# Kernel tuning notes

Measured on AMD Instinct MI355X. Metric: run time of the kernel, lower is better.

The kernel has to match this reference:

```python
import jax, jax.numpy as jnp
import numpy as np

N, E, DIM, H = 50000, 800000, 64, 2
HD = H * DIM


def setup_inputs() -> dict:
    key = jax.random.key(0)
    ks = jax.random.split(key, 16)
    s = 0.05
    return {
        "x": jax.random.normal(ks[0], (N, DIM), jnp.float32),
        "edge_index": jax.random.randint(ks[1], (2, E), 0, N, jnp.int64),
        "Wq": jax.random.normal(ks[2], (DIM, HD), jnp.float32) * s,
        "bq": jax.random.normal(ks[3], (HD,), jnp.float32) * s,
        "Wk": jax.random.normal(ks[4], (DIM, HD), jnp.float32) * s,
        "bk": jax.random.normal(ks[5], (HD,), jnp.float32) * s,
        "Wv": jax.random.normal(ks[6], (DIM, HD), jnp.float32) * s,
        "bv": jax.random.normal(ks[7], (HD,), jnp.float32) * s,
        "Wskip": jax.random.normal(ks[8], (DIM, HD), jnp.float32) * s,
        "bskip": jax.random.normal(ks[9], (HD,), jnp.float32) * s,
        "Wc": jax.random.normal(ks[10], (HD, DIM), jnp.float32) * s,
        "bc": jax.random.normal(ks[11], (DIM,), jnp.float32) * s,
        "gamma": jnp.ones((DIM,), jnp.float32),
        "beta": jnp.zeros((DIM,), jnp.float32),
    }


def reference(x, edge_index, Wq, bq, Wk, bk, Wv, bv, Wskip, bskip, Wc, bc, gamma, beta):
    src, dst = edge_index[0], edge_index[1]  # messages flow src -> dst
    # TransformerConv: per-head q/k/v projections, [N, H, D]
    q = (x @ Wq + bq).reshape(N, H, DIM)
    k = (x @ Wk + bk).reshape(N, H, DIM)
    v = (x @ Wv + bv).reshape(N, H, DIM)
    scale = 1.0 / np.sqrt(DIM).astype(np.float32)
    # edge-wise attention logits: [E, H]
    alpha = jnp.einsum('ehd,ehd->eh', q[dst], k[src]) * scale
    # segment softmax over incoming edges of each dst node (PyG softmax)
    amax = jax.ops.segment_max(alpha, dst, num_segments=N)
    a = jnp.exp(alpha - amax[dst])
    asum = jax.ops.segment_sum(a, dst, num_segments=N)
    a = a / (asum[dst] + 1e-16)
    # weighted scatter-aggregate of values: [N, H, D] -> concat heads
    out = jax.ops.segment_sum(a[:, :, None] * v[src], dst, num_segments=N)
    out = out.reshape(N, HD)
    # root/skip connection (root_weight=True default)
    out = out + (x @ Wskip + bskip)
    # concat linear: H*D -> dim
    out = out @ Wc + bc
    # pyg.LayerNorm default mode='graph': normalize over ALL nodes+features
    out = out - out.mean()
    out = out / (out.std() + 1e-5)  # std with unbiased=False (jnp default ddof=0)
    return out * gamma + beta
```

## Files before the change

kernel.cpp:

```cpp
#include <hip/hip_runtime.h>
#include <hip/hip_bf16.h>

#define N_NODES 50000
#define N_EDGES 800000
#define DIM 64
#define NHEAD 2
#define HD 128
#define NCOL 448
#define MAXDEG 64

#define NBIN 196
#define BCAP 6144
#define ACH 2048
#define BIN_BLKS 391

#define PREP_B 112
#define PROJ_B 782

#define QSCALE 0.18033688011112042f

typedef short bf16x8 __attribute__((ext_vector_type(8)));
typedef float f32x16 __attribute__((ext_vector_type(16)));
typedef float f32x2 __attribute__((ext_vector_type(2)));

__device__ __forceinline__ unsigned short f2bf(float f) {
    unsigned u = __float_as_uint(f);
    unsigned r = (u + 0x7fffu + ((u >> 16) & 1u)) >> 16;
    return (unsigned short)r;
}
__device__ __forceinline__ unsigned char f2fp8(float f) {
    int r = __builtin_amdgcn_cvt_pk_fp8_f32(f, f, 0, false);
    return (unsigned char)(r & 0xff);
}

__global__ __launch_bounds__(256) void k_pb(
    const int* __restrict__ ei,
    const float* __restrict__ Wq, const float* __restrict__ bq,
    const float* __restrict__ Wk, const float* __restrict__ bk,
    const float* __restrict__ Wv, const float* __restrict__ bv,
    const float* __restrict__ Wskip, const float* __restrict__ bskip,
    const float* __restrict__ Wc, const float* __restrict__ bc,
    unsigned short* __restrict__ WallT, float* __restrict__ ball,
    int* __restrict__ bincnt, unsigned* __restrict__ bins,
    double* __restrict__ sacc)
{
    const int t = threadIdx.x;
    if (blockIdx.x < PREP_B) {
        if (blockIdx.x == 0) { sacc[t] = 0.0; sacc[256 + t] = 0.0; }
        int gid = blockIdx.x * 256 + t;
        const int j = gid >> 6;
        const int d = gid & 63;
        float w, bb;
        if (j < 128) {
            w = Wq[d * HD + j] * QSCALE;
            bb = bq[j] * QSCALE;
        } else if (j < 256) {
            int jj = j - 128;
            w = Wk[d * HD + jj];
            bb = bk[jj];
        } else if (j < 384) {
            int jj = j - 256;
            int h = jj >> 6, jc = jj & 63;
            float s = 0.f, sb = 0.f;
            for (int c = 0; c < 64; c++) {
                float wc = Wc[(h * 64 + c) * DIM + jc];
                s  += Wv[d * HD + h * 64 + c] * wc;
                sb += bv[h * 64 + c] * wc;
            }
            w = s; bb = sb;
        } else {
            int jj = j - 384;
            float s = 0.f, sb = bc[jj];
            for (int c = 0; c < HD; c++) {
                float wc = Wc[c * DIM + jj];
                s  += Wskip[d * HD + c] * wc;
                sb += bskip[c] * wc;
            }
            w = s; bb = sb;
        }
        WallT[gid] = f2bf(w);
        if (d == 0) ball[j] = bb;
        return;
    }
    __shared__ int hist[256];
    __shared__ int gbase[256];
    const int e0 = (blockIdx.x - PREP_B) * ACH;
    hist[t] = 0;
    __syncthreads();
    unsigned pk8[8];
    int bin8[8], sl8[8];
#pragma unroll
    for (int k = 0; k < 8; k++) {
        int e = e0 + t + k * 256;
        if (e < N_EDGES) {
            int src = ei[e];
            int d = ei[N_EDGES + e];
            int bin = d >> 8;
            pk8[k] = (unsigned)(((d & 255) << 16) | src);
            bin8[k] = bin;
            sl8[k] = atomicAdd(&hist[bin], 1);
        } else {
            bin8[k] = -1;
        }
    }
    __syncthreads();
    if (t < NBIN) {
        int h = hist[t];
        if (h > 0) gbase[t] = atomicAdd(&bincnt[t], h);
    }
    __syncthreads();
#pragma unroll
    for (int k = 0; k < 8; k++) {
        int bin = bin8[k];
        if (bin >= 0) {
            int pos = gbase[bin] + sl8[k];
            if (pos < BCAP) bins[(size_t)bin * BCAP + pos] = pk8[k];
        }
    }
}

__global__ __launch_bounds__(256) void k_ep(
    const float* __restrict__ x,
    const unsigned short* __restrict__ WallT, const float* __restrict__ ball,
    float* __restrict__ q, unsigned char* __restrict__ kv, float* __restrict__ skipc,
    const int* __restrict__ bincnt, const unsigned* __restrict__ bins,
    int* __restrict__ deg, unsigned short* __restrict__ elist)
{
    __shared__ __align__(16) unsigned char smem[65536];
    const int blk = blockIdx.x;
    const int t = threadIdx.x;
    if (blk >= PROJ_B) {
        const int bin = blk - PROJ_B;
        int* nodecnt = (int*)smem;
        nodecnt[t] = 0;
        __syncthreads();
        int cnt = bincnt[bin]; if (cnt > BCAP) cnt = BCAP;
        const unsigned* bp = bins + (size_t)bin * BCAP;
        for (int i = t; i < cnt; i += 256) {
            unsigned p = bp[i];
            int local = p >> 16;
            int src = p & 0xffff;
            int sl = atomicAdd(&nodecnt[local], 1);
            if (sl < MAXDEG)
                elist[((size_t)((bin << 8) | local)) * MAXDEG + sl] = (unsigned short)src;
        }
        __syncthreads();
        int node = (bin << 8) + t;
        if (node < N_NODES) {
            int dgv = nodecnt[t];
            deg[node] = dgv > MAXDEG ? MAXDEG : dgv;
        }
        return;
    }
    float* q_s = (float*)smem;
    unsigned char* kv_s = smem + 32768;
    float* sk_s = (float*)(smem + 49152);

    const int w = t >> 6;
    const int lane = t & 63;
    const int col = lane & 31;
    const int khalf = lane >> 5;
    const int nloc0 = (w >> 1) * 32;
    const int n0 = blk * 64 + nloc0;
    const int ct0 = (w & 1) * 7;
    const int rowbase = 4 * khalf;

    int nread = n0 + col; if (nread >= N_NODES) nread = N_NODES - 1;
    const float* ap = x + (size_t)nread * 64 + khalf * 8;
    bf16x8 afrag[4];
#pragma unroll
    for (int kk = 0; kk < 4; kk++) {
        float4 xa = *((const float4*)(ap + kk * 16));
        float4 xb4 = *((const float4*)(ap + kk * 16 + 4));
        bf16x8 f;
        f[0] = (short)f2bf(xa.x); f[1] = (short)f2bf(xa.y);
        f[2] = (short)f2bf(xa.z); f[3] = (short)f2bf(xa.w);
        f[4] = (short)f2bf(xb4.x); f[5] = (short)f2bf(xb4.y);
        f[6] = (short)f2bf(xb4.z); f[7] = (short)f2bf(xb4.w);
        afrag[kk] = f;
    }

    for (int tt = 0; tt < 7; tt++) {
        const int gc = (ct0 + tt) * 32 + col;
        const float b = ball[gc];
        f32x16 acc;
#pragma unroll
        for (int r = 0; r < 16; r++) acc[r] = b;
        const unsigned short* bp = WallT + (size_t)gc * 64 + khalf * 8;
#pragma unroll
        for (int kk = 0; kk < 4; kk++) {
            bf16x8 bfrag = *((const bf16x8*)(bp + kk * 16));
            acc = __builtin_amdgcn_mfma_f32_32x32x16_bf16(afrag[kk], bfrag, acc, 0, 0, 0);
        }
        if (gc < 128) {
#pragma unroll
            for (int r = 0; r < 16; r++) {
                int nl = nloc0 + rowbase + (r & 3) + 8 * (r >> 2);
                q_s[nl * 128 + gc] = acc[r];
            }
        } else if (gc < 384) {
            int ch = gc - 128;
            int half = ch >> 7;
            int cc = ch & 127;
            int h = cc >> 6, c = cc & 63;
            int pos = half * 128 + ((c >> 3) << 4) + (h << 3) + (c & 7);
#pragma unroll
            for (int r = 0; r < 16; r++) {
                int nl = nloc0 + rowbase + (r & 3) + 8 * (r >> 2);
                kv_s[nl * 256 + pos] = f2fp8(acc[r]);
            }
        } else {
            int c = gc - 384;
#pragma unroll
            for (int r = 0; r < 16; r++) {
                int nl = nloc0 + rowbase + (r & 3) + 8 * (r >> 2);
                sk_s[nl * 64 + c] = acc[r];
            }
        }
    }
    __syncthreads();
    const size_t nbase = (size_t)blk * 64;
    const int nrem = (int)(N_NODES - nbase);
    {
        const float4* s4 = (const float4*)q_s;
        float4* g4 = (float4*)(q + nbase * HD);
        int lim = nrem >= 64 ? 2048 : nrem * 32;
#pragma unroll
        for (int kk = 0; kk < 8; kk++) {
            int i = t + kk * 256;
            if (i < lim) g4[i] = s4[i];
        }
    }
    {
        const uint4* s4 = (const uint4*)kv_s;
        uint4* g4 = (uint4*)(kv + nbase * 256);
        int lim = nrem >= 64 ? 1024 : nrem * 16;
#pragma unroll
        for (int kk = 0; kk < 4; kk++) {
            int i = t + kk * 256;
            if (i < lim) g4[i] = s4[i];
        }
    }
    {
        const float4* s4 = (const float4*)sk_s;
        float4* g4 = (float4*)(skipc + nbase * DIM);
        int lim = nrem >= 64 ? 1024 : nrem * 16;
#pragma unroll
        for (int kk = 0; kk < 4; kk++) {
            int i = t + kk * 256;
            if (i < lim) g4[i] = s4[i];
        }
    }
}

__global__ __launch_bounds__(256) void k_attn(
    const float* __restrict__ q, const unsigned char* __restrict__ kv,
    const float* __restrict__ skipc,
    const int* __restrict__ deg, const unsigned short* __restrict__ elist,
    float* __restrict__ out, double* __restrict__ sacc)
{
    const int w = threadIdx.x >> 6;
    const int lane = threadIdx.x & 63;
    const int g = lane >> 3;
    const int j = lane & 7;
    const int n = blockIdx.x * 4 + w;
    const float4* qp4 = (const float4*)(q + (size_t)n * HD);
    const float4 qa = qp4[2 * j],      qb = qp4[2 * j + 1];
    const float4 qc = qp4[16 + 2 * j], qd = qp4[17 + 2 * j];
    f32x2 q0[4], q1[4];
    q0[0] = (f32x2){qa.x, qa.y}; q0[1] = (f32x2){qa.z, qa.w};
    q0[2] = (f32x2){qb.x, qb.y}; q0[3] = (f32x2){qb.z, qb.w};
    q1[0] = (f32x2){qc.x, qc.y}; q1[1] = (f32x2){qc.z, qc.w};
    q1[2] = (f32x2){qd.x, qd.y}; q1[3] = (f32x2){qd.z, qd.w};
    const int myE = elist[(size_t)n * MAXDEG + lane];
    float4 sa = {0,0,0,0}, sb = {0,0,0,0};
    if (g == 0) {
        const float4* sk = (const float4*)(skipc + (size_t)n * DIM);
        sa = sk[2 * j]; sb = sk[2 * j + 1];
    }
    f32x2 acc0[4], acc1[4];
#pragma unroll
    for (int i = 0; i < 4; i++) {
        acc0[i] = (f32x2){0.f, 0.f};
        acc1[i] = (f32x2){0.f, 0.f};
    }
    float l0 = 0.f, l1 = 0.f;
    int dg = deg[n]; if (dg > MAXDEG) dg = MAXDEG;
    for (int b0 = 0; b0 < dg; b0 += 8) {
        int idx = b0 + g;
        bool valid = idx < dg;
        int s = __shfl(myE, valid ? idx : 0, 64);
        const uint4* kp = (const uint4*)(kv + (size_t)s * 256);
        uint4 K = kp[j];
        uint4 V = kp[8 + j];
        f32x2 p0v = q0[0] * __builtin_amdgcn_cvt_pk_f32_fp8(K.x, false);
        p0v += q0[1] * __builtin_amdgcn_cvt_pk_f32_fp8(K.x, true);
        p0v += q0[2] * __builtin_amdgcn_cvt_pk_f32_fp8(K.y, false);
        p0v += q0[3] * __builtin_amdgcn_cvt_pk_f32_fp8(K.y, true);
        f32x2 p1v = q1[0] * __builtin_amdgcn_cvt_pk_f32_fp8(K.z, false);
        p1v += q1[1] * __builtin_amdgcn_cvt_pk_f32_fp8(K.z, true);
        p1v += q1[2] * __builtin_amdgcn_cvt_pk_f32_fp8(K.w, false);
        p1v += q1[3] * __builtin_amdgcn_cvt_pk_f32_fp8(K.w, true);
        float p0 = p0v[0] + p0v[1];
        float p1 = p1v[0] + p1v[1];
#pragma unroll
        for (int off = 1; off < 8; off <<= 1) {
            p0 += __shfl_xor(p0, off, 64);
            p1 += __shfl_xor(p1, off, 64);
        }
        float w0 = valid ? __builtin_amdgcn_exp2f(p0) : 0.f;
        float w1 = valid ? __builtin_amdgcn_exp2f(p1) : 0.f;
        l0 += w0; l1 += w1;
        f32x2 w0v = {w0, w0}, w1v = {w1, w1};
        acc0[0] += w0v * __builtin_amdgcn_cvt_pk_f32_fp8(V.x, false);
        acc0[1] += w0v * __builtin_amdgcn_cvt_pk_f32_fp8(V.x, true);
        acc0[2] += w0v * __builtin_amdgcn_cvt_pk_f32_fp8(V.y, false);
        acc0[3] += w0v * __builtin_amdgcn_cvt_pk_f32_fp8(V.y, true);
        acc1[0] += w1v * __builtin_amdgcn_cvt_pk_f32_fp8(V.z, false);
        acc1[1] += w1v * __builtin_amdgcn_cvt_pk_f32_fp8(V.z, true);
        acc1[2] += w1v * __builtin_amdgcn_cvt_pk_f32_fp8(V.w, false);
        acc1[3] += w1v * __builtin_amdgcn_cvt_pk_f32_fp8(V.w, true);
    }
    float* a0 = (float*)acc0;
    float* a1 = (float*)acc1;
#pragma unroll
    for (int off = 8; off < 64; off <<= 1) {
        l0 += __shfl_xor(l0, off, 64);
        l1 += __shfl_xor(l1, off, 64);
#pragma unroll
        for (int i = 0; i < 8; i++) {
            a0[i] += __shfl_xor(a0[i], off, 64);
            a1[i] += __shfl_xor(a1[i], off, 64);
        }
    }
    if (g == 0) {
        float inv0 = 1.f / (l0 + 1e-16f), inv1 = 1.f / (l1 + 1e-16f);
        float o[8];
        o[0] = a0[0] * inv0 + a1[0] * inv1 + sa.x;
        o[1] = a0[1] * inv0 + a1[1] * inv1 + sa.y;
        o[2] = a0[2] * inv0 + a1[2] * inv1 + sa.z;
        o[3] = a0[3] * inv0 + a1[3] * inv1 + sa.w;
        o[4] = a0[4] * inv0 + a1[4] * inv1 + sb.x;
        o[5] = a0[5] * inv0 + a1[5] * inv1 + sb.y;
        o[6] = a0[6] * inv0 + a1[6] * inv1 + sb.z;
        o[7] = a0[7] * inv0 + a1[7] * inv1 + sb.w;
        float4 r0 = {o[0], o[1], o[2], o[3]}, r1 = {o[4], o[5], o[6], o[7]};
        float4* op = (float4*)(out + (size_t)n * DIM);
        op[2 * j] = r0; op[2 * j + 1] = r1;
        float s_ = 0.f, ss = 0.f;
#pragma unroll
        for (int i = 0; i < 8; i++) { s_ += o[i]; ss += o[i] * o[i]; }
#pragma unroll
        for (int off = 1; off < 8; off <<= 1) {
            s_ += __shfl_xor(s_, off, 64);
            ss += __shfl_xor(ss, off, 64);
        }
        if (j == 0) {
            int slot = n & 255;
            atomicAdd(&sacc[slot], (double)s_);
            atomicAdd(&sacc[256 + slot], (double)ss);
        }
    }
}

__global__ __launch_bounds__(256) void k_norm(
    float* __restrict__ out, const double* __restrict__ sacc,
    const float* __restrict__ gamma, const float* __restrict__ beta)
{
    const int t = threadIdx.x;
    __shared__ double red[8];
    double s = sacc[t];
    double ss = sacc[256 + t];
#pragma unroll
    for (int off = 32; off > 0; off >>= 1) {
        s  += __shfl_down(s, off);
        ss += __shfl_down(ss, off);
    }
    int wv = t >> 6;
    if ((t & 63) == 0) { red[wv * 2] = s; red[wv * 2 + 1] = ss; }
    __syncthreads();
    double S  = red[0] + red[2] + red[4] + red[6];
    double SS = red[1] + red[3] + red[5] + red[7];
    const double cnt = (double)N_NODES * (double)DIM;
    double mean = S / cnt;
    double var  = SS / cnt - mean * mean;
    if (var < 0.0) var = 0.0;
    float mf = (float)mean;
    float inv = 1.0f / ((float)sqrt(var) + 1e-5f);
    int i = blockIdx.x * 256 + t;
    if (i >= N_NODES * DIM / 4) return;
    float4 v = ((const float4*)out)[i];
    float4 gv = ((const float4*)gamma)[i & 15];
    float4 bv2 = ((const float4*)beta)[i & 15];
    v.x = (v.x - mf) * inv * gv.x + bv2.x;
    v.y = (v.y - mf) * inv * gv.y + bv2.y;
    v.z = (v.z - mf) * inv * gv.z + bv2.z;
    v.w = (v.w - mf) * inv * gv.w + bv2.w;
    ((float4*)out)[i] = v;
}

extern "C" void kernel_launch(void* const* d_in, const int* in_sizes, int n_in,
                              void* d_out, int out_size, void* d_ws, size_t ws_size,
                              hipStream_t stream) {
    const float* x     = (const float*)d_in[0];
    const int*   ei    = (const int*)d_in[1];
    const float* Wq    = (const float*)d_in[2];
    const float* bq    = (const float*)d_in[3];
    const float* Wk    = (const float*)d_in[4];
    const float* bk    = (const float*)d_in[5];
    const float* Wv    = (const float*)d_in[6];
    const float* bv    = (const float*)d_in[7];
    const float* Wsk   = (const float*)d_in[8];
    const float* bsk   = (const float*)d_in[9];
    const float* Wc    = (const float*)d_in[10];
    const float* bc    = (const float*)d_in[11];
    const float* gamma = (const float*)d_in[12];
    const float* beta  = (const float*)d_in[13];
    float* out = (float*)d_out;

    double* sacc = (double*)d_ws;
    float* ws = (float*)(sacc + 512);
    const size_t NF = (size_t)N_NODES * HD;
    float* q = ws;
    unsigned char* kv = (unsigned char*)(ws + NF);
    float* skipc = (float*)(kv + (size_t)N_NODES * 256);
    unsigned short* WallT = (unsigned short*)(skipc + (size_t)N_NODES * DIM);
    float* ball   = (float*)(WallT + NCOL * 64);
    int* bincnt   = (int*)(ball + NCOL);
    unsigned* bins = (unsigned*)(bincnt + 256);
    int* deg      = (int*)(bins + (size_t)NBIN * BCAP);
    unsigned short* elist = (unsigned short*)(deg + N_NODES);

    hipMemsetAsync(bincnt, 0, 256 * sizeof(int), stream);
    hipLaunchKernelGGL(k_pb, dim3(PREP_B + BIN_BLKS), dim3(256), 0, stream,
                       ei, Wq, bq, Wk, bk, Wv, bv, Wsk, bsk, Wc, bc,
                       WallT, ball, bincnt, bins, sacc);
    hipLaunchKernelGGL(k_ep, dim3(PROJ_B + NBIN), dim3(256), 0, stream,
                       x, WallT, ball, q, kv, skipc, bincnt, bins, deg, elist);
    hipLaunchKernelGGL(k_attn, dim3(N_NODES / 4), dim3(256), 0, stream,
                       q, kv, skipc, deg, elist, out, sacc);
    hipLaunchKernelGGL(k_norm, dim3(N_NODES * DIM / 4 / 256 + 1), dim3(256), 0, stream,
                       out, sacc, gamma, beta);
}
```

Measured before the change: 187.1 us.

## Map one node per 8-lane group in attention instead of one node per wavefront

The attention kernel now assigns each 8-lane group its own destination node, so a wavefront handles 8 nodes and each group walks that node's edges sequentially. Before, a wavefront handled one node with its 8 groups splitting the edges. This removes the cross-group shuffle reduction of the accumulators and the idle lanes in the epilogue. Edge indices are loaded as a uint4 per lane and extracted per step. The cost is that each wavefront loops to the maximum degree among its 8 nodes, so degree imbalance wastes work, and there is less memory-level parallelism per node.

```diff
diff --git a/kernel.cpp b/kernel.cpp
--- a/kernel.cpp
+++ b/kernel.cpp
@@ -16,6 +16,7 @@
 
 #define PREP_B 112
 #define PROJ_B 782
+#define ATTN_B 1563
 
 #define QSCALE 0.18033688011112042f
 
@@ -263,8 +264,21 @@
     const int lane = threadIdx.x & 63;
     const int g = lane >> 3;
     const int j = lane & 7;
-    const int n = blockIdx.x * 4 + w;
-    const float4* qp4 = (const float4*)(q + (size_t)n * HD);
+    const int n = blockIdx.x * 32 + w * 8 + g;
+    const bool nvalid = n < N_NODES;
+    const int nn = nvalid ? n : N_NODES - 1;
+
+    const uint4 E = *((const uint4*)(elist + (size_t)nn * MAXDEG + j * 8));
+    int dg = nvalid ? deg[nn] : 0;
+    if (dg > MAXDEG) dg = MAXDEG;
+    int dgmax = dg;
+#pragma unroll
+    for (int off = 8; off < 64; off <<= 1) {
+        int o = __shfl_xor(dgmax, off, 64);
+        dgmax = o > dgmax ? o : dgmax;
+    }
+
+    const float4* qp4 = (const float4*)(q + (size_t)nn * HD);
     const float4 qa = qp4[2 * j],      qb = qp4[2 * j + 1];
     const float4 qc = qp4[16 + 2 * j], qd = qp4[17 + 2 * j];
     f32x2 q0[4], q1[4];
@@ -272,12 +286,7 @@
     q0[2] = (f32x2){qb.x, qb.y}; q0[3] = (f32x2){qb.z, qb.w};
     q1[0] = (f32x2){qc.x, qc.y}; q1[1] = (f32x2){qc.z, qc.w};
     q1[2] = (f32x2){qd.x, qd.y}; q1[3] = (f32x2){qd.z, qd.w};
-    const int myE = elist[(size_t)n * MAXDEG + lane];
-    float4 sa = {0,0,0,0}, sb = {0,0,0,0};
-    if (g == 0) {
-        const float4* sk = (const float4*)(skipc + (size_t)n * DIM);
-        sa = sk[2 * j]; sb = sk[2 * j + 1];
-    }
+
     f32x2 acc0[4], acc1[4];
 #pragma unroll
     for (int i = 0; i < 4; i++) {
@@ -285,14 +294,18 @@
         acc1[i] = (f32x2){0.f, 0.f};
     }
     float l0 = 0.f, l1 = 0.f;
-    int dg = deg[n]; if (dg > MAXDEG) dg = MAXDEG;
-    for (int b0 = 0; b0 < dg; b0 += 8) {
-        int idx = b0 + g;
-        bool valid = idx < dg;
-        int s = __shfl(myE, valid ? idx : 0, 64);
+
+    for (int k = 0; k < dgmax; ++k) {
+        const bool valid = k < dg;
+        const int hw = k & 7;
+        unsigned dwd = (hw < 4) ? ((hw < 2) ? E.x : E.y)
+                                : ((hw < 6) ? E.z : E.w);
+        unsigned v16 = (hw & 1) ? (dwd >> 16) : (dwd & 0xffffu);
+        int s = __shfl((int)v16, (lane & 56) | (k >> 3), 64);
+        if (!valid) s = 0;
         const uint4* kp = (const uint4*)(kv + (size_t)s * 256);
-        uint4 K = kp[j];
-        uint4 V = kp[8 + j];
+        const uint4 K = kp[j];
+        const uint4 V = kp[8 + j];
         f32x2 p0v = q0[0] * __builtin_amdgcn_cvt_pk_f32_fp8(K.x, false);
         p0v += q0[1] * __builtin_amdgcn_cvt_pk_f32_fp8(K.x, true);
         p0v += q0[2] * __builtin_amdgcn_cvt_pk_f32_fp8(K.y, false);
@@ -321,45 +334,40 @@
         acc1[2] += w1v * __builtin_amdgcn_cvt_pk_f32_fp8(V.w, false);
         acc1[3] += w1v * __builtin_amdgcn_cvt_pk_f32_fp8(V.w, true);
     }
+
+    const float inv0 = 1.f / (l0 + 1e-16f), inv1 = 1.f / (l1 + 1e-16f);
+    const float4* sk = (const float4*)(skipc + (size_t)nn * DIM);
+    const float4 sa = sk[2 * j], sb = sk[2 * j + 1];
     float* a0 = (float*)acc0;
     float* a1 = (float*)acc1;
-#pragma unroll
-    for (int off = 8; off < 64; off <<= 1) {
-        l0 += __shfl_xor(l0, off, 64);
-        l1 += __shfl_xor(l1, off, 64);
-#pragma unroll
-        for (int i = 0; i < 8; i++) {
-            a0[i] += __shfl_xor(a0[i], off, 64);
-            a1[i] += __shfl_xor(a1[i], off, 64);
-        }
-    }
-    if (g == 0) {
-        float inv0 = 1.f / (l0 + 1e-16f), inv1 = 1.f / (l1 + 1e-16f);
-        float o[8];
-        o[0] = a0[0] * inv0 + a1[0] * inv1 + sa.x;
-        o[1] = a0[1] * inv0 + a1[1] * inv1 + sa.y;
-        o[2] = a0[2] * inv0 + a1[2] * inv1 + sa.z;
-        o[3] = a0[3] * inv0 + a1[3] * inv1 + sa.w;
-        o[4] = a0[4] * inv0 + a1[4] * inv1 + sb.x;
-        o[5] = a0[5] * inv0 + a1[5] * inv1 + sb.y;
-        o[6] = a0[6] * inv0 + a1[6] * inv1 + sb.z;
-        o[7] = a0[7] * inv0 + a1[7] * inv1 + sb.w;
+    float o[8];
+    o[0] = a0[0] * inv0 + a1[0] * inv1 + sa.x;
+    o[1] = a0[1] * inv0 + a1[1] * inv1 + sa.y;
+    o[2] = a0[2] * inv0 + a1[2] * inv1 + sa.z;
+    o[3] = a0[3] * inv0 + a1[3] * inv1 + sa.w;
+    o[4] = a0[4] * inv0 + a1[4] * inv1 + sb.x;
+    o[5] = a0[5] * inv0 + a1[5] * inv1 + sb.y;
+    o[6] = a0[6] * inv0 + a1[6] * inv1 + sb.z;
+    o[7] = a0[7] * inv0 + a1[7] * inv1 + sb.w;
+    if (nvalid) {
         float4 r0 = {o[0], o[1], o[2], o[3]}, r1 = {o[4], o[5], o[6], o[7]};
         float4* op = (float4*)(out + (size_t)n * DIM);
         op[2 * j] = r0; op[2 * j + 1] = r1;
-        float s_ = 0.f, ss = 0.f;
+    }
+    float s_ = 0.f, ss = 0.f;
+    if (nvalid) {
 #pragma unroll
         for (int i = 0; i < 8; i++) { s_ += o[i]; ss += o[i] * o[i]; }
-#pragma unroll
-        for (int off = 1; off < 8; off <<= 1) {
-            s_ += __shfl_xor(s_, off, 64);
-            ss += __shfl_xor(ss, off, 64);
-        }
-        if (j == 0) {
-            int slot = n & 255;
-            atomicAdd(&sacc[slot], (double)s_);
-            atomicAdd(&sacc[256 + slot], (double)ss);
-        }
+    }
+#pragma unroll
+    for (int off = 1; off < 64; off <<= 1) {
+        s_ += __shfl_xor(s_, off, 64);
+        ss += __shfl_xor(ss, off, 64);
+    }
+    if (lane == 0) {
+        int slot = (blockIdx.x * 4 + w) & 255;
+        atomicAdd(&sacc[slot], (double)s_);
+        atomicAdd(&sacc[256 + slot], (double)ss);
     }
 }
 
@@ -437,7 +445,7 @@
                        WallT, ball, bincnt, bins, sacc);
     hipLaunchKernelGGL(k_ep, dim3(PROJ_B + NBIN), dim3(256), 0, stream,
                        x, WallT, ball, q, kv, skipc, bincnt, bins, deg, elist);
-    hipLaunchKernelGGL(k_attn, dim3(N_NODES / 4), dim3(256), 0, stream,
+    hipLaunchKernelGGL(k_attn, dim3(ATTN_B), dim3(256), 0, stream,
                        q, kv, skipc, deg, elist, out, sacc);
     hipLaunchKernelGGL(k_norm, dim3(N_NODES * DIM / 4 / 256 + 1), dim3(256), 0, stream,
                        out, sacc, gamma, beta);
```

Result: faster. 177.0 us (-5.4%).
